# Performance work log

Hardware: AMD Instinct MI355X
Metric: run time of the kernel (lower is better)

Reference implementation:

```python
import jax, jax.numpy as jnp
from jax import lax
import numpy as np

ALPHA = 2.0
EROSIONS = 10


def setup_inputs() -> dict:
    key = jax.random.key(0)
    k1, k2 = jax.random.split(key)
    b, c, h, w = 32, 1, 1024, 1024
    pred = jax.random.uniform(k1, (b, c, h, w), dtype=jnp.float32)
    target = jax.random.randint(k2, (b, c, h, w), 0, 2, dtype=jnp.int32)
    return {"pred": pred, "target": target}


def _perform_erosion(bound, kernel, alpha, erosions):
    # bound: (b, 1, H, W); kernel: (1, 1, 3, 3) cross * 0.2
    def step(carry, k):
        bnd, eroted = carry
        dilation = lax.conv_general_dilated(bnd, kernel, window_strides=(1, 1), padding="SAME")
        erosion = jnp.maximum(dilation - 0.5, 0.0)
        # per-sample global max/min over channel+spatial dims
        emax = jnp.max(erosion, axis=(1, 2, 3), keepdims=True)
        emin = jnp.min(erosion, axis=(1, 2, 3), keepdims=True)
        denom = emax - emin
        safe = jnp.where(denom != 0, denom, jnp.ones_like(denom))
        erosion = jnp.where(denom != 0, (erosion - emin) / safe, erosion)
        eroted = eroted + erosion * (k + 1.0) ** alpha
        return (erosion, eroted), None

    init = (bound, jnp.zeros_like(bound))
    (_, eroted), _ = lax.scan(step, init, jnp.arange(erosions, dtype=bound.dtype))
    return eroted


def reference(pred, target):
    # cross-shaped 3x3 erosion kernel scaled by 0.2 (fixed buffer)
    cross = jnp.array([[0.0, 1.0, 0.0], [1.0, 1.0, 1.0], [0.0, 1.0, 0.0]], dtype=pred.dtype) * 0.2
    kernel = cross[None, None]  # (1, 1, 3, 3)
    c = pred.shape[1]
    losses = []
    for i in range(c):
        tgt = (target == i).astype(pred.dtype)  # (b, c, H, W); c==1 here
        bound = (pred[:, i : i + 1] - tgt) ** 2
        eroted = _perform_erosion(bound, kernel, ALPHA, EROSIONS)
        losses.append(jnp.mean(eroted))
    return jnp.mean(jnp.stack(losses))
```

## Files before the change

### kernel.cpp

```cpp
#include <hip/hip_runtime.h>
#include <hip/hip_fp16.h>

#define BATCH 32
#define H 1024
#define W 1024
#define NPIX (H * W)
#define ITERS 10
#define SROWS 16
#define BROWS 32
#define STRIPS (H / BROWS)

typedef _Float16 half8_t __attribute__((ext_vector_type(8)));

struct Stats {
    unsigned maxbits[ITERS][BATCH];
    unsigned minbits[ITERS][BATCH];
    double   sum[ITERS][BATCH];
};

__global__ void init_stats(Stats* st) {
    int i = blockIdx.x * blockDim.x + threadIdx.x;
    if (i < ITERS * BATCH) {
        (&st->maxbits[0][0])[i] = 0u;
        (&st->minbits[0][0])[i] = 0x7f800000u;
        (&st->sum[0][0])[i]     = 0.0;
    }
}

__device__ __forceinline__ float bound1(const float* __restrict__ pred,
                                        const int* __restrict__ tgt, size_t off) {
    float d = pred[off] - (tgt[off] == 0 ? 1.f : 0.f);
    return d * d;
}

template <int MODE>
__device__ __forceinline__ void row_load8(
    const float* __restrict__ pred, const int* __restrict__ target,
    const _Float16* __restrict__ in, size_t base, int r, int lane128,
    float emin, float invd, float f[8], float& L, float& R)
{
    const int  col = lane128 * 8;
    const bool inb = (r >= 0) && (r < H);
    size_t off = base + (size_t)r * W + col;
    if (inb) {
        if (MODE == 0) {
            float4 p0 = *(const float4*)(pred + off);
            float4 p1 = *(const float4*)(pred + off + 4);
            int4   t0 = *(const int4*)(target + off);
            int4   t1 = *(const int4*)(target + off + 4);
            float d;
            d = p0.x - (t0.x == 0 ? 1.f : 0.f); f[0] = d * d;
            d = p0.y - (t0.y == 0 ? 1.f : 0.f); f[1] = d * d;
            d = p0.z - (t0.z == 0 ? 1.f : 0.f); f[2] = d * d;
            d = p0.w - (t0.w == 0 ? 1.f : 0.f); f[3] = d * d;
            d = p1.x - (t1.x == 0 ? 1.f : 0.f); f[4] = d * d;
            d = p1.y - (t1.y == 0 ? 1.f : 0.f); f[5] = d * d;
            d = p1.z - (t1.z == 0 ? 1.f : 0.f); f[6] = d * d;
            d = p1.w - (t1.w == 0 ? 1.f : 0.f); f[7] = d * d;
        } else {
            half8_t x = *(const half8_t*)(in + off);
            #pragma unroll
            for (int j = 0; j < 8; ++j)
                f[j] = ((float)x[j] - emin) * invd;
        }
    } else {
        #pragma unroll
        for (int j = 0; j < 8; ++j) f[j] = 0.f;
    }

    L = __shfl_up(f[7], 1, 64);
    R = __shfl_down(f[0], 1, 64);

    const int wl = lane128 & 63;
    if (!inb) { L = 0.f; R = 0.f; return; }
    if (lane128 == 0) {
        L = 0.f;
    } else if (wl == 0) {
        size_t o = off - 1;
        L = (MODE == 0) ? bound1(pred, target, o)
                        : ((float)in[o] - emin) * invd;
    }
    if (lane128 == 127) {
        R = 0.f;
    } else if (wl == 63) {
        size_t o = off + 8;
        R = (MODE == 0) ? bound1(pred, target, o)
                        : ((float)in[o] - emin) * invd;
    }
}

template <int MODE, int STORE>
__global__ __launch_bounds__(256) void erode_strip(
    const float* __restrict__ pred, const int* __restrict__ target,
    const _Float16* __restrict__ in, _Float16* __restrict__ out,
    Stats* __restrict__ st, int iter)
{
    const int blk = blockIdx.x;
    const int b   = blk >> 5;
    const int s   = blk & (STRIPS - 1);
    const int tid = threadIdx.x;
    const int sub     = tid >> 7;
    const int lane128 = tid & 127;
    const int r0  = s * BROWS + sub * SROWS;
    const int col = lane128 * 8;
    const size_t base = (size_t)b * NPIX;

    float emin = 0.f, invd = 1.f;
    if (MODE == 1) {
        float emax = __uint_as_float(st->maxbits[iter - 1][b]);
        float emn  = __uint_as_float(st->minbits[iter - 1][b]);
        float denom = emax - emn;
        if (denom != 0.f) { emin = emn; invd = 1.f / denom; }
    }

    float prev[8], cur[8], nxt[8];
    float Lp, Rp, Lc, Rc, Ln, Rn;
    row_load8<MODE>(pred, target, in, base, r0 - 1, lane128, emin, invd, prev, Lp, Rp);
    row_load8<MODE>(pred, target, in, base, r0,     lane128, emin, invd, cur,  Lc, Rc);

    float  m  = 0.f;
    float  mn = __builtin_inf();
    double sum = 0.0;

    #pragma unroll 2
    for (int i = 0; i < SROWS; ++i) {
        const int r = r0 + i;
        row_load8<MODE>(pred, target, in, base, r + 1, lane128, emin, invd, nxt, Ln, Rn);

        float e[8];
        #pragma unroll
        for (int j = 0; j < 8; ++j) {
            float lf = (j == 0) ? Lc : cur[j - 1];
            float rf = (j == 7) ? Rc : cur[j + 1];
            e[j] = fmaxf(0.2f * (cur[j] + lf + rf + prev[j] + nxt[j]) - 0.5f, 0.f);
        }

        if (STORE) {
            half8_t o;
            #pragma unroll
            for (int j = 0; j < 8; ++j) o[j] = (_Float16)e[j];
            *(half8_t*)(out + base + (size_t)r * W + col) = o;
        }

        float rm = fmaxf(fmaxf(fmaxf(e[0], e[1]), fmaxf(e[2], e[3])),
                         fmaxf(fmaxf(e[4], e[5]), fmaxf(e[6], e[7])));
        float rn = fminf(fminf(fminf(e[0], e[1]), fminf(e[2], e[3])),
                         fminf(fminf(e[4], e[5]), fminf(e[6], e[7])));
        float rs = ((e[0] + e[1]) + (e[2] + e[3])) + ((e[4] + e[5]) + (e[6] + e[7]));
        m   = fmaxf(m, rm);
        mn  = fminf(mn, rn);
        sum += (double)rs;

        #pragma unroll
        for (int j = 0; j < 8; ++j) { prev[j] = cur[j]; cur[j] = nxt[j]; }
        Lc = Ln; Rc = Rn;
    }

    #pragma unroll
    for (int off = 32; off > 0; off >>= 1) {
        m   = fmaxf(m,  __shfl_down(m,  off, 64));
        mn  = fminf(mn, __shfl_down(mn, off, 64));
        sum += __shfl_down(sum, off, 64);
    }
    __shared__ float  smax[4];
    __shared__ float  smin[4];
    __shared__ double ssum[4];
    int lane = tid & 63, wave = tid >> 6;
    if (lane == 0) { smax[wave] = m; smin[wave] = mn; ssum[wave] = sum; }
    __syncthreads();
    if (tid == 0) {
        m   = fmaxf(fmaxf(smax[0], smax[1]), fmaxf(smax[2], smax[3]));
        mn  = fminf(fminf(smin[0], smin[1]), fminf(smin[2], smin[3]));
        sum = ssum[0] + ssum[1] + ssum[2] + ssum[3];
        atomicMax(&st->maxbits[iter][b], __float_as_uint(m));
        atomicMin(&st->minbits[iter][b], __float_as_uint(mn));
        atomicAdd(&st->sum[iter][b], sum);
    }
}

__global__ void finalize(const Stats* __restrict__ st, float* __restrict__ out) {
    if (threadIdx.x == 0 && blockIdx.x == 0) {
        double total = 0.0;
        for (int k = 0; k < ITERS; ++k) {
            double w = (double)((k + 1) * (k + 1));
            for (int b = 0; b < BATCH; ++b) {
                float emax  = __uint_as_float(st->maxbits[k][b]);
                float emn   = __uint_as_float(st->minbits[k][b]);
                float denom = emax - emn;
                double s = st->sum[k][b];
                double sn;
                if (denom != 0.f)
                    sn = (s - (double)NPIX * (double)emn) / (double)denom;
                else
                    sn = s;
                total += w * sn;
            }
        }
        out[0] = (float)(total / ((double)BATCH * (double)NPIX));
    }
}

extern "C" void kernel_launch(void* const* d_in, const int* in_sizes, int n_in,
                              void* d_out, int out_size, void* d_ws, size_t ws_size,
                              hipStream_t stream) {
    (void)in_sizes; (void)n_in; (void)out_size;
    const float* pred   = (const float*)d_in[0];
    const int*   target = (const int*)d_in[1];

    const size_t fieldBytes = (size_t)BATCH * NPIX * sizeof(_Float16);
    char* ws = (char*)d_ws;
    _Float16* bufA;
    _Float16* bufB;
    Stats* st;
    if (ws_size >= 2 * fieldBytes + sizeof(Stats)) {
        bufA = (_Float16*)ws;
        bufB = (_Float16*)(ws + fieldBytes);
        st   = (Stats*)(ws + 2 * fieldBytes);
    } else {
        bufA = (_Float16*)ws;
        bufB = (_Float16*)d_in[1];
        st   = (Stats*)(ws + fieldBytes);
    }

    init_stats<<<1, 320, 0, stream>>>(st);

    dim3 grid(BATCH * STRIPS), block(256);
    erode_strip<0, 1><<<grid, block, 0, stream>>>(pred, target, nullptr, bufA, st, 0);

    _Float16* src = bufA;
    _Float16* dst = bufB;
    for (int k = 1; k < ITERS; ++k) {
        if (k == ITERS - 1)
            erode_strip<1, 0><<<grid, block, 0, stream>>>(nullptr, nullptr, src, dst, st, k);
        else
            erode_strip<1, 1><<<grid, block, 0, stream>>>(nullptr, nullptr, src, dst, st, k);
        _Float16* t = src; src = dst; dst = t;
    }

    finalize<<<1, 64, 0, stream>>>(st, (float*)d_out);
}
```

Before: 581.8 us.

## Map one wave per full row with 16 pixels per lane and prefetch rows

Each thread now processes 16 contiguous pixels, so a single 64-lane wave covers a whole 1024-wide row. The wave-edge halo loads from global memory go away and the horizontal neighbours come only from shuffles. Each wave handles 8 rows instead of 16, and the mid kernels software-prefetch raw fp16 rows one row ahead of the stencil. The kernels are specialized into init and mid variants with launch bounds of 4 blocks, trading more registers per thread for fewer branches and better load overlap.

```diff
diff --git a/kernel.cpp b/kernel.cpp
--- a/kernel.cpp
+++ b/kernel.cpp
@@ -1,14 +1,14 @@
 #include <hip/hip_runtime.h>
-#include <hip/hip_fp16.h>
 
 #define BATCH 32
 #define H 1024
 #define W 1024
 #define NPIX (H * W)
 #define ITERS 10
-#define SROWS 16
+#define SROWS 8
 #define BROWS 32
 #define STRIPS (H / BROWS)
+#define PX 16
 
 typedef _Float16 half8_t __attribute__((ext_vector_type(8)));
 
@@ -27,135 +27,54 @@
     }
 }
 
-__device__ __forceinline__ float bound1(const float* __restrict__ pred,
-                                        const int* __restrict__ tgt, size_t off) {
-    float d = pred[off] - (tgt[off] == 0 ? 1.f : 0.f);
-    return d * d;
-}
-
-template <int MODE>
-__device__ __forceinline__ void row_load8(
-    const float* __restrict__ pred, const int* __restrict__ target,
-    const _Float16* __restrict__ in, size_t base, int r, int lane128,
-    float emin, float invd, float f[8], float& L, float& R)
-{
-    const int  col = lane128 * 8;
-    const bool inb = (r >= 0) && (r < H);
-    size_t off = base + (size_t)r * W + col;
+__device__ __forceinline__ void fetch_raw(const _Float16* __restrict__ in,
+                                          size_t rowbase, int colo,
+                                          half8_t& a, half8_t& b) {
+    const _Float16* p = in + rowbase + colo;
+    a = *(const half8_t*)p;
+    b = *(const half8_t*)(p + 8);
+}
+
+__device__ __forceinline__ void norm16(float f[PX], half8_t a, half8_t b,
+                                       float emin, float invd, bool inb) {
     if (inb) {
-        if (MODE == 0) {
-            float4 p0 = *(const float4*)(pred + off);
-            float4 p1 = *(const float4*)(pred + off + 4);
-            int4   t0 = *(const int4*)(target + off);
-            int4   t1 = *(const int4*)(target + off + 4);
-            float d;
-            d = p0.x - (t0.x == 0 ? 1.f : 0.f); f[0] = d * d;
-            d = p0.y - (t0.y == 0 ? 1.f : 0.f); f[1] = d * d;
-            d = p0.z - (t0.z == 0 ? 1.f : 0.f); f[2] = d * d;
-            d = p0.w - (t0.w == 0 ? 1.f : 0.f); f[3] = d * d;
-            d = p1.x - (t1.x == 0 ? 1.f : 0.f); f[4] = d * d;
-            d = p1.y - (t1.y == 0 ? 1.f : 0.f); f[5] = d * d;
-            d = p1.z - (t1.z == 0 ? 1.f : 0.f); f[6] = d * d;
-            d = p1.w - (t1.w == 0 ? 1.f : 0.f); f[7] = d * d;
-        } else {
-            half8_t x = *(const half8_t*)(in + off);
-            #pragma unroll
-            for (int j = 0; j < 8; ++j)
-                f[j] = ((float)x[j] - emin) * invd;
+        #pragma unroll
+        for (int j = 0; j < 8; ++j) {
+            f[j]     = ((float)a[j] - emin) * invd;
+            f[j + 8] = ((float)b[j] - emin) * invd;
         }
     } else {
         #pragma unroll
-        for (int j = 0; j < 8; ++j) f[j] = 0.f;
-    }
-
-    L = __shfl_up(f[7], 1, 64);
-    R = __shfl_down(f[0], 1, 64);
-
-    const int wl = lane128 & 63;
-    if (!inb) { L = 0.f; R = 0.f; return; }
-    if (lane128 == 0) {
-        L = 0.f;
-    } else if (wl == 0) {
-        size_t o = off - 1;
-        L = (MODE == 0) ? bound1(pred, target, o)
-                        : ((float)in[o] - emin) * invd;
-    }
-    if (lane128 == 127) {
-        R = 0.f;
-    } else if (wl == 63) {
-        size_t o = off + 8;
-        R = (MODE == 0) ? bound1(pred, target, o)
-                        : ((float)in[o] - emin) * invd;
-    }
-}
-
-template <int MODE, int STORE>
-__global__ __launch_bounds__(256) void erode_strip(
-    const float* __restrict__ pred, const int* __restrict__ target,
-    const _Float16* __restrict__ in, _Float16* __restrict__ out,
-    Stats* __restrict__ st, int iter)
-{
-    const int blk = blockIdx.x;
-    const int b   = blk >> 5;
-    const int s   = blk & (STRIPS - 1);
+        for (int j = 0; j < PX; ++j) f[j] = 0.f;
+    }
+}
+
+__device__ __forceinline__ void bound16(const float* __restrict__ pred,
+                                        const int* __restrict__ tgt,
+                                        size_t rowbase, int colo, bool inb,
+                                        float f[PX]) {
+    if (!inb) {
+        #pragma unroll
+        for (int j = 0; j < PX; ++j) f[j] = 0.f;
+        return;
+    }
+    const size_t off = rowbase + colo;
+    #pragma unroll
+    for (int q = 0; q < 4; ++q) {
+        float4 p = *(const float4*)(pred + off + 4 * q);
+        int4   t = *(const int4*)(tgt + off + 4 * q);
+        float d;
+        d = p.x - (t.x == 0 ? 1.f : 0.f); f[4 * q + 0] = d * d;
+        d = p.y - (t.y == 0 ? 1.f : 0.f); f[4 * q + 1] = d * d;
+        d = p.z - (t.z == 0 ? 1.f : 0.f); f[4 * q + 2] = d * d;
+        d = p.w - (t.w == 0 ? 1.f : 0.f); f[4 * q + 3] = d * d;
+    }
+}
+
+__device__ __forceinline__ void block_stats(float m, float mn, double sum,
+                                            Stats* __restrict__ st, int iter, int b) {
     const int tid = threadIdx.x;
-    const int sub     = tid >> 7;
-    const int lane128 = tid & 127;
-    const int r0  = s * BROWS + sub * SROWS;
-    const int col = lane128 * 8;
-    const size_t base = (size_t)b * NPIX;
-
-    float emin = 0.f, invd = 1.f;
-    if (MODE == 1) {
-        float emax = __uint_as_float(st->maxbits[iter - 1][b]);
-        float emn  = __uint_as_float(st->minbits[iter - 1][b]);
-        float denom = emax - emn;
-        if (denom != 0.f) { emin = emn; invd = 1.f / denom; }
-    }
-
-    float prev[8], cur[8], nxt[8];
-    float Lp, Rp, Lc, Rc, Ln, Rn;
-    row_load8<MODE>(pred, target, in, base, r0 - 1, lane128, emin, invd, prev, Lp, Rp);
-    row_load8<MODE>(pred, target, in, base, r0,     lane128, emin, invd, cur,  Lc, Rc);
-
-    float  m  = 0.f;
-    float  mn = __builtin_inf();
-    double sum = 0.0;
-
-    #pragma unroll 2
-    for (int i = 0; i < SROWS; ++i) {
-        const int r = r0 + i;
-        row_load8<MODE>(pred, target, in, base, r + 1, lane128, emin, invd, nxt, Ln, Rn);
-
-        float e[8];
-        #pragma unroll
-        for (int j = 0; j < 8; ++j) {
-            float lf = (j == 0) ? Lc : cur[j - 1];
-            float rf = (j == 7) ? Rc : cur[j + 1];
-            e[j] = fmaxf(0.2f * (cur[j] + lf + rf + prev[j] + nxt[j]) - 0.5f, 0.f);
-        }
-
-        if (STORE) {
-            half8_t o;
-            #pragma unroll
-            for (int j = 0; j < 8; ++j) o[j] = (_Float16)e[j];
-            *(half8_t*)(out + base + (size_t)r * W + col) = o;
-        }
-
-        float rm = fmaxf(fmaxf(fmaxf(e[0], e[1]), fmaxf(e[2], e[3])),
-                         fmaxf(fmaxf(e[4], e[5]), fmaxf(e[6], e[7])));
-        float rn = fminf(fminf(fminf(e[0], e[1]), fminf(e[2], e[3])),
-                         fminf(fminf(e[4], e[5]), fminf(e[6], e[7])));
-        float rs = ((e[0] + e[1]) + (e[2] + e[3])) + ((e[4] + e[5]) + (e[6] + e[7]));
-        m   = fmaxf(m, rm);
-        mn  = fminf(mn, rn);
-        sum += (double)rs;
-
-        #pragma unroll
-        for (int j = 0; j < 8; ++j) { prev[j] = cur[j]; cur[j] = nxt[j]; }
-        Lc = Ln; Rc = Rn;
-    }
-
+    const int lane = tid & 63, wave = tid >> 6;
     #pragma unroll
     for (int off = 32; off > 0; off >>= 1) {
         m   = fmaxf(m,  __shfl_down(m,  off, 64));
@@ -165,7 +84,6 @@
     __shared__ float  smax[4];
     __shared__ float  smin[4];
     __shared__ double ssum[4];
-    int lane = tid & 63, wave = tid >> 6;
     if (lane == 0) { smax[wave] = m; smin[wave] = mn; ssum[wave] = sum; }
     __syncthreads();
     if (tid == 0) {
@@ -178,6 +96,139 @@
     }
 }
 
+__global__ __launch_bounds__(256, 4) void erode_init(
+    const float* __restrict__ pred, const int* __restrict__ target,
+    _Float16* __restrict__ out, Stats* __restrict__ st)
+{
+    const int blk = blockIdx.x;
+    const int b   = blk >> 5;
+    const int s   = blk & (STRIPS - 1);
+    const int tid = threadIdx.x;
+    const int wave = tid >> 6, lane = tid & 63;
+    const int r0  = s * BROWS + wave * SROWS;
+    const int colo = lane * PX;
+    const size_t base = (size_t)b * NPIX;
+
+    float prev[PX], cur[PX], nxt[PX];
+    bound16(pred, target, base + (size_t)(r0 - 1) * W, colo, r0 > 0, prev);
+    bound16(pred, target, base + (size_t)r0 * W,       colo, true,   cur);
+
+    float  m  = 0.f;
+    float  mn = __uint_as_float(0x7f800000u);
+    double sum = 0.0;
+
+    #pragma unroll
+    for (int i = 0; i < SROWS; ++i) {
+        const int rn = r0 + i + 1;
+        bound16(pred, target, base + (size_t)rn * W, colo, rn < H, nxt);
+
+        float L = __shfl_up(cur[PX - 1], 1, 64);
+        float R = __shfl_down(cur[0], 1, 64);
+        if (lane == 0)  L = 0.f;
+        if (lane == 63) R = 0.f;
+
+        half8_t o0, o1;
+        float rs = 0.f;
+        #pragma unroll
+        for (int j = 0; j < PX; ++j) {
+            float lf = j ? cur[j - 1] : L;
+            float rf = (j < PX - 1) ? cur[j + 1] : R;
+            float e  = fmaxf(0.2f * (cur[j] + lf + rf + prev[j] + nxt[j]) - 0.5f, 0.f);
+            if (j < 8) o0[j] = (_Float16)e; else o1[j - 8] = (_Float16)e;
+            m = fmaxf(m, e); mn = fminf(mn, e); rs += e;
+        }
+        sum += (double)rs;
+
+        _Float16* op = out + base + (size_t)(r0 + i) * W + colo;
+        *(half8_t*)op = o0;
+        *(half8_t*)(op + 8) = o1;
+
+        #pragma unroll
+        for (int j = 0; j < PX; ++j) { prev[j] = cur[j]; cur[j] = nxt[j]; }
+    }
+
+    block_stats(m, mn, sum, st, 0, b);
+}
+
+template <int STORE>
+__global__ __launch_bounds__(256, 4) void erode_mid(
+    const _Float16* __restrict__ in, _Float16* __restrict__ out,
+    Stats* __restrict__ st, int iter)
+{
+    const int blk = blockIdx.x;
+    const int b   = blk >> 5;
+    const int s   = blk & (STRIPS - 1);
+    const int tid = threadIdx.x;
+    const int wave = tid >> 6, lane = tid & 63;
+    const int r0  = s * BROWS + wave * SROWS;
+    const int colo = lane * PX;
+    const size_t base = (size_t)b * NPIX;
+
+    float emin = 0.f, invd = 1.f;
+    {
+        float emax  = __uint_as_float(st->maxbits[iter - 1][b]);
+        float emn   = __uint_as_float(st->minbits[iter - 1][b]);
+        float denom = emax - emn;
+        if (denom != 0.f) { emin = emn; invd = 1.f / denom; }
+    }
+
+    float prev[PX], cur[PX], nxt[PX];
+    {
+        half8_t ta = {}, tb = {};
+        bool inb = (r0 > 0);
+        if (inb) fetch_raw(in, base + (size_t)(r0 - 1) * W, colo, ta, tb);
+        norm16(prev, ta, tb, emin, invd, inb);
+    }
+    {
+        half8_t ta, tb;
+        fetch_raw(in, base + (size_t)r0 * W, colo, ta, tb);
+        norm16(cur, ta, tb, emin, invd, true);
+    }
+    half8_t ra = {}, rb = {};
+    half8_t pa = {}, pb = {};
+    if (r0 + 1 < H) fetch_raw(in, base + (size_t)(r0 + 1) * W, colo, ra, rb);
+
+    float  m  = 0.f;
+    float  mn = __uint_as_float(0x7f800000u);
+    double sum = 0.0;
+
+    #pragma unroll
+    for (int i = 0; i < SROWS; ++i) {
+        if ((i < SROWS - 1) && (r0 + i + 2 < H))
+            fetch_raw(in, base + (size_t)(r0 + i + 2) * W, colo, pa, pb);
+        norm16(nxt, ra, rb, emin, invd, r0 + i + 1 < H);
+
+        float L = __shfl_up(cur[PX - 1], 1, 64);
+        float R = __shfl_down(cur[0], 1, 64);
+        if (lane == 0)  L = 0.f;
+        if (lane == 63) R = 0.f;
+
+        half8_t o0, o1;
+        float rs = 0.f;
+        #pragma unroll
+        for (int j = 0; j < PX; ++j) {
+            float lf = j ? cur[j - 1] : L;
+            float rf = (j < PX - 1) ? cur[j + 1] : R;
+            float e  = fmaxf(0.2f * (cur[j] + lf + rf + prev[j] + nxt[j]) - 0.5f, 0.f);
+            if (j < 8) o0[j] = (_Float16)e; else o1[j - 8] = (_Float16)e;
+            m = fmaxf(m, e); mn = fminf(mn, e); rs += e;
+        }
+        sum += (double)rs;
+
+        if (STORE) {
+            _Float16* op = out + base + (size_t)(r0 + i) * W + colo;
+            *(half8_t*)op = o0;
+            *(half8_t*)(op + 8) = o1;
+        }
+
+        #pragma unroll
+        for (int j = 0; j < PX; ++j) { prev[j] = cur[j]; cur[j] = nxt[j]; }
+        ra = pa; rb = pb;
+    }
+
+    block_stats(m, mn, sum, st, iter, b);
+}
+
 __global__ void finalize(const Stats* __restrict__ st, float* __restrict__ out) {
     if (threadIdx.x == 0 && blockIdx.x == 0) {
         double total = 0.0;
@@ -187,12 +238,12 @@
                 float emax  = __uint_as_float(st->maxbits[k][b]);
                 float emn   = __uint_as_float(st->minbits[k][b]);
                 float denom = emax - emn;
-                double s = st->sum[k][b];
+                double ssv = st->sum[k][b];
                 double sn;
                 if (denom != 0.f)
-                    sn = (s - (double)NPIX * (double)emn) / (double)denom;
+                    sn = (ssv - (double)NPIX * (double)emn) / (double)denom;
                 else
-                    sn = s;
+                    sn = ssv;
                 total += w * sn;
             }
         }
@@ -225,15 +276,15 @@
     init_stats<<<1, 320, 0, stream>>>(st);
 
     dim3 grid(BATCH * STRIPS), block(256);
-    erode_strip<0, 1><<<grid, block, 0, stream>>>(pred, target, nullptr, bufA, st, 0);
+    erode_init<<<grid, block, 0, stream>>>(pred, target, bufA, st);
 
     _Float16* src = bufA;
     _Float16* dst = bufB;
     for (int k = 1; k < ITERS; ++k) {
         if (k == ITERS - 1)
-            erode_strip<1, 0><<<grid, block, 0, stream>>>(nullptr, nullptr, src, dst, st, k);
+            erode_mid<0><<<grid, block, 0, stream>>>(src, dst, st, k);
         else
-            erode_strip<1, 1><<<grid, block, 0, stream>>>(nullptr, nullptr, src, dst, st, k);
+            erode_mid<1><<<grid, block, 0, stream>>>(src, dst, st, k);
         _Float16* t = src; src = dst; dst = t;
     }
 
```

Measured after the change: 734.0 us. 1.26x slower.
